# Kernel optimization log

Hardware: AMD Instinct MI355X
Metric: run time of the kernel (lower is better)

Reference implementation:

```python
import jax, jax.numpy as jnp
import numpy as np

B, H, LQ, LK, D = 2, 16, 2048, 2048, 128

def setup_inputs() -> dict:
    key = jax.random.key(0)
    k1, k2, k3 = jax.random.split(key, 3)
    q = jax.random.normal(k1, (B, H, LQ, D), dtype=jnp.float32)
    k = jax.random.normal(k2, (B, H, LK, D), dtype=jnp.float32)
    v = jax.random.normal(k3, (B, H, LK, D), dtype=jnp.float32)
    return {"q": q, "k": k, "v": v}

def reference(q, k, v):
    # scaled dot-product attention: softmax(q k^T / sqrt(D)) v
    scale = q.shape[-1] ** (-0.5)
    # scores: [B,H,Lq,Lk]
    scores = jnp.einsum('bhqd,bhkd->bhqk', q, k) * scale
    attn = jax.nn.softmax(scores, axis=-1)
    out = jnp.einsum('bhqk,bhkd->bhqd', attn, v)  # [B,H,Lq,Dv]
    return out
```

## Files before the change

kernel.cpp:

```cpp
#include <hip/hip_runtime.h>
#include <hip/hip_bf16.h>
#include <cstdint>

#define LQ_N   2048
#define LK_N   2048
#define DD     128
#define NHEADS 32
#define QBLK   128
#define KVBLK  64
#define NKV    (LK_N / KVBLK)
#define NQB    (LQ_N / QBLK)
#define SCALE  0.08838834764831845f
#define SCALE2 0.1275525003267101f

#define KTILE_BYTES (KVBLK * DD * 2)
#define WS_K_BYTES  ((size_t)NHEADS * NKV * KTILE_BYTES)
#define WS_NEED     (2 * WS_K_BYTES)

#define PSTR 72

typedef __attribute__((ext_vector_type(8)))  short bf16x8;
typedef __attribute__((ext_vector_type(4)))  float f32x4;
typedef __attribute__((ext_vector_type(16))) float f32x16;

#if __has_builtin(__builtin_amdgcn_exp2f)
#define EXP2F __builtin_amdgcn_exp2f
#else
#define EXP2F exp2f
#endif

#define MFMA32(a, b, c) __builtin_amdgcn_mfma_f32_32x32x16_bf16((a), (b), (c), 0, 0, 0)

__device__ inline unsigned short f2bf(float f) {
    union { float f; unsigned u; } x; x.f = f;
    unsigned r = (x.u + 0x7fffu + ((x.u >> 16) & 1u)) >> 16;
    return (unsigned short)r;
}

__device__ inline unsigned cvt_pk_bf16(float lo, float hi) {
    unsigned r;
    asm("v_cvt_pk_bf16_f32 %0, %1, %2" : "=v"(r) : "v"(lo), "v"(hi));
    return r;
}

__device__ inline float fmax4(float a, float b, float c, float d) {
    return fmaxf(fmaxf(a, b), fmaxf(c, d));
}

__device__ inline bf16x8 make_pfrag(float v0, float v1, float v2, float v3,
                                    float v4, float v5, float v6, float v7) {
    unsigned a0 = cvt_pk_bf16(v0, v1);
    unsigned a1 = cvt_pk_bf16(v2, v3);
    unsigned b0 = cvt_pk_bf16(v4, v5);
    unsigned b1 = cvt_pk_bf16(v6, v7);
    asm("v_permlane32_swap_b32 %0, %1" : "+v"(a0), "+v"(b0));
    asm("v_permlane32_swap_b32 %0, %1" : "+v"(a1), "+v"(b1));
    union { unsigned u[4]; bf16x8 v8; } u;
    u.u[0] = a0; u.u[1] = a1; u.u[2] = b0; u.u[3] = b1;
    return u.v8;
}

__device__ inline void gld16(const char* g, const char* l) {
    __builtin_amdgcn_global_load_lds(
        (const __attribute__((address_space(1))) unsigned int*)g,
        (__attribute__((address_space(3))) unsigned int*)l,
        16, 0, 0);
}

__global__ __launch_bounds__(256, 2)
void prep_k_kernel(const float* __restrict__ K, char* __restrict__ ws)
{
    __shared__ unsigned short kt[KVBLK * 136];
    const int tid  = threadIdx.x;
    const int kvt  = blockIdx.x;
    const int head = blockIdx.y;
    const float* Kh = K + ((size_t)head * LK_N + (size_t)kvt * KVBLK) * DD;
    #pragma unroll
    for (int i = 0; i < 4; ++i) {
        int c = tid + 256 * i;
        int r  = c >> 4;
        int c8 = c & 15;
        const float* src = Kh + (size_t)r * DD + c8 * 8;
        float4 a = *(const float4*)src;
        float4 b = *(const float4*)(src + 4);
        bf16x8 t;
        t[0] = (short)f2bf(a.x * SCALE2); t[1] = (short)f2bf(a.y * SCALE2);
        t[2] = (short)f2bf(a.z * SCALE2); t[3] = (short)f2bf(a.w * SCALE2);
        t[4] = (short)f2bf(b.x * SCALE2); t[5] = (short)f2bf(b.y * SCALE2);
        t[6] = (short)f2bf(b.z * SCALE2); t[7] = (short)f2bf(b.w * SCALE2);
        *(bf16x8*)&kt[r * 136 + c8 * 8] = t;
    }
    __syncthreads();
    char* dst = ws + ((size_t)head * NKV + kvt) * KTILE_BYTES;
    #pragma unroll
    for (int i = 0; i < 4; ++i) {
        int c = tid + 256 * i;
        int g = c >> 6;
        int r = c & 63;
        bf16x8 t = *(const bf16x8*)&kt[r * 136 + g * 8];
        *(bf16x8*)(dst + c * 16) = t;
    }
}

__global__ __launch_bounds__(256, 2)
void prep_vt_kernel(const float* __restrict__ V, char* __restrict__ ws)
{
    __shared__ unsigned short vt[DD * PSTR];
    const int tid  = threadIdx.x;
    const int kvt  = blockIdx.x;
    const int head = blockIdx.y;
    const float* Vh = V + ((size_t)head * LK_N + (size_t)kvt * KVBLK) * DD;
    #pragma unroll
    for (int i = 0; i < 8; ++i) {
        int f = tid + 256 * i;
        int r  = f >> 5;
        int c4 = f & 31;
        float4 x = *(const float4*)(Vh + (size_t)r * DD + c4 * 4);
        vt[(c4 * 4 + 0) * PSTR + r] = f2bf(x.x);
        vt[(c4 * 4 + 1) * PSTR + r] = f2bf(x.y);
        vt[(c4 * 4 + 2) * PSTR + r] = f2bf(x.z);
        vt[(c4 * 4 + 3) * PSTR + r] = f2bf(x.w);
    }
    __syncthreads();
    char* dst = ws + WS_K_BYTES + ((size_t)head * NKV + kvt) * KTILE_BYTES;
    #pragma unroll
    for (int i = 0; i < 4; ++i) {
        int c = tid + 256 * i;
        int g = c >> 7;
        int d = c & 127;
        bf16x8 t = *(const bf16x8*)&vt[d * PSTR + g * 8];
        *(bf16x8*)(dst + c * 16) = t;
    }
}

#define LOADVF(a0, a1, a2, a3, KS) { \
    a0 = *(const bf16x8*)(vtile + (((2 * (KS) + h) * 128 +  0 + l31) << 4)); \
    a1 = *(const bf16x8*)(vtile + (((2 * (KS) + h) * 128 + 32 + l31) << 4)); \
    a2 = *(const bf16x8*)(vtile + (((2 * (KS) + h) * 128 + 64 + l31) << 4)); \
    a3 = *(const bf16x8*)(vtile + (((2 * (KS) + h) * 128 + 96 + l31) << 4)); }

#define PV_ROUND(S, B, a0, a1, a2, a3) { \
    float e0 = EXP2F(S[B + 0] - m_run), e1 = EXP2F(S[B + 1] - m_run); \
    float e2 = EXP2F(S[B + 2] - m_run), e3 = EXP2F(S[B + 3] - m_run); \
    float e4 = EXP2F(S[B + 4] - m_run), e5 = EXP2F(S[B + 5] - m_run); \
    float e6 = EXP2F(S[B + 6] - m_run), e7 = EXP2F(S[B + 7] - m_run); \
    sum += ((e0 + e1) + (e2 + e3)) + ((e4 + e5) + (e6 + e7)); \
    bf16x8 pf = make_pfrag(e0, e1, e2, e3, e4, e5, e6, e7); \
    __builtin_amdgcn_s_setprio(1); \
    o_acc[0] = MFMA32(a0, pf, o_acc[0]); \
    o_acc[1] = MFMA32(a1, pf, o_acc[1]); \
    o_acc[2] = MFMA32(a2, pf, o_acc[2]); \
    o_acc[3] = MFMA32(a3, pf, o_acc[3]); \
    __builtin_amdgcn_s_setprio(0); }

__global__ __launch_bounds__(256, 2)
void attn_main_kernel(const float* __restrict__ Q, const char* __restrict__ kws,
                      const char* __restrict__ vws, float* __restrict__ O)
{
    __shared__ bf16x8 kbuf[3][KTILE_BYTES / 16];

    const int tid  = threadIdx.x;
    const int lane = tid & 63;
    const int wave = tid >> 6;
    const int l31  = lane & 31;
    const int h    = lane >> 5;

    const int bid  = blockIdx.x;
    const int sid  = (bid & 7) * (NQB * NHEADS / 8) + (bid >> 3);
    const int head = sid >> 4;
    const int qb   = sid & 15;

    const float* Qh = Q + (size_t)head * LQ_N * DD;
    float*       Oh = O + (size_t)head * LQ_N * DD;
    const char*  kt_g = kws + (size_t)head * NKV * KTILE_BYTES;
    const char*  vt_g = vws + (size_t)head * NKV * KTILE_BYTES;

    const int qrow = qb * QBLK + wave * 32 + l31;
    bf16x8 qf[8];
    {
        const float* qp = Qh + (size_t)qrow * DD + 8 * h;
        #pragma unroll
        for (int kd = 0; kd < 8; ++kd) {
            float4 a = *(const float4*)(qp + 16 * kd);
            float4 b = *(const float4*)(qp + 16 * kd + 4);
            bf16x8 t;
            t[0] = (short)f2bf(a.x); t[1] = (short)f2bf(a.y);
            t[2] = (short)f2bf(a.z); t[3] = (short)f2bf(a.w);
            t[4] = (short)f2bf(b.x); t[5] = (short)f2bf(b.y);
            t[6] = (short)f2bf(b.z); t[7] = (short)f2bf(b.w);
            qf[kd] = t;
        }
    }
    asm volatile("s_waitcnt vmcnt(0)" ::: "memory");

    f32x16 o_acc[4];
    #pragma unroll
    for (int nt = 0; nt < 4; ++nt)
        #pragma unroll
        for (int i = 0; i < 16; ++i) o_acc[nt][i] = 0.f;
    float m_run = -1e30f, l_run = 0.f;

    auto issue_k = [&](int t) {
        const char* ks = kt_g + (size_t)t * KTILE_BYTES;
        const char* kl = (const char*)&kbuf[t % 3][0];
        #pragma unroll
        for (int i = 0; i < 4; ++i) {
            int off = (tid + 256 * i) * 16;
            gld16(ks + off, kl + off);
        }
    };

    issue_k(0);
    issue_k(1);

    for (int t = 0; t < NKV; ++t) {
        const char* vtile = vt_g + (size_t)t * KTILE_BYTES;
        bf16x8 vA0, vA1, vA2, vA3, vB0, vB1, vB2, vB3;

        LOADVF(vA0, vA1, vA2, vA3, 0);

        if (t < NKV - 1) asm volatile("s_waitcnt vmcnt(8)" ::: "memory");
        else             asm volatile("s_waitcnt vmcnt(4)" ::: "memory");
        __builtin_amdgcn_s_barrier();
        __builtin_amdgcn_sched_barrier(0);

        if (t + 2 < NKV) issue_k(t + 2);

        const char* kb = (const char*)&kbuf[t % 3][0];

        f32x16 s0, s1;
        #pragma unroll
        for (int i = 0; i < 16; ++i) { s0[i] = 0.f; s1[i] = 0.f; }
        __builtin_amdgcn_s_setprio(1);
        #pragma unroll
        for (int kd = 0; kd < 8; ++kd) {
            bf16x8 kf0 = *(const bf16x8*)(kb + (((2 * kd + h) * 64 + l31) << 4));
            bf16x8 kf1 = *(const bf16x8*)(kb + (((2 * kd + h) * 64 + 32 + l31) << 4));
            s0 = MFMA32(kf0, qf[kd], s0);
            s1 = MFMA32(kf1, qf[kd], s1);
        }
        __builtin_amdgcn_s_setprio(0);

        float x0 = fmax4(s0[0],  s0[1],  s0[2],  s0[3]);
        float x1 = fmax4(s0[4],  s0[5],  s0[6],  s0[7]);
        float x2 = fmax4(s0[8],  s0[9],  s0[10], s0[11]);
        float x3 = fmax4(s0[12], s0[13], s0[14], s0[15]);
        float y0 = fmax4(s1[0],  s1[1],  s1[2],  s1[3]);
        float y1 = fmax4(s1[4],  s1[5],  s1[6],  s1[7]);
        float y2 = fmax4(s1[8],  s1[9],  s1[10], s1[11]);
        float y3 = fmax4(s1[12], s1[13], s1[14], s1[15]);
        float pm = fmaxf(fmaxf(fmaxf(x0, x1), fmaxf(x2, x3)),
                         fmaxf(fmaxf(y0, y1), fmaxf(y2, y3)));
        pm = fmaxf(pm, __shfl_xor(pm, 32));

        if (!__all(pm <= m_run + 8.0f)) {
            float mn = fmaxf(m_run, pm);
            float al = EXP2F(m_run - mn);
            m_run = mn;
            l_run *= al;
            #pragma unroll
            for (int nt = 0; nt < 4; ++nt)
                #pragma unroll
                for (int i = 0; i < 16; ++i) o_acc[nt][i] *= al;
        }

        float sum = 0.f;
        LOADVF(vB0, vB1, vB2, vB3, 1);
        PV_ROUND(s0, 0, vA0, vA1, vA2, vA3);
        LOADVF(vA0, vA1, vA2, vA3, 2);
        PV_ROUND(s0, 8, vB0, vB1, vB2, vB3);
        LOADVF(vB0, vB1, vB2, vB3, 3);
        PV_ROUND(s1, 0, vA0, vA1, vA2, vA3);
        PV_ROUND(s1, 8, vB0, vB1, vB2, vB3);

        sum += __shfl_xor(sum, 32);
        l_run += sum;
    }

    float inv = 1.0f / l_run;
    float* op = Oh + (size_t)qrow * DD;
    #pragma unroll
    for (int nt = 0; nt < 4; ++nt)
        #pragma unroll
        for (int p = 0; p < 4; ++p) {
            int dbase = 32 * nt + 8 * p + 4 * h;
            float4 w;
            w.x = o_acc[nt][4 * p + 0] * inv;
            w.y = o_acc[nt][4 * p + 1] * inv;
            w.z = o_acc[nt][4 * p + 2] * inv;
            w.w = o_acc[nt][4 * p + 3] * inv;
            *(float4*)(op + dbase) = w;
        }
}

#define KSTRIDE  136
#define VTSTRIDE 40
#define FKV 32

__global__ __launch_bounds__(256, 2)
void attn_fwd_fallback(const float* __restrict__ Q, const float* __restrict__ K,
                       const float* __restrict__ V, float* __restrict__ O)
{
    __shared__ unsigned short k_lds[FKV * KSTRIDE];
    __shared__ unsigned short vt_lds[DD * VTSTRIDE];
    __shared__ unsigned short p_lds2[4 * 16 * VTSTRIDE];

    const int tid  = threadIdx.x;
    const int lane = tid & 63;
    const int wave = tid >> 6;
    const int head = blockIdx.y;
    const int qb   = blockIdx.x;

    const float* Qh = Q + (size_t)head * LQ_N * DD;
    const float* Kh = K + (size_t)head * LK_N * DD;
    const float* Vh = V + (size_t)head * LK_N * DD;
    float*       Oh = O + (size_t)head * LQ_N * DD;

    const int r16 = lane & 15;
    const int g   = lane >> 4;

    const int qrow = qb * 64 + wave * 16 + r16;
    bf16x8 qf[4];
    {
        const float* qp = Qh + (size_t)qrow * DD + 8 * g;
        #pragma unroll
        for (int kt = 0; kt < 4; ++kt) {
            float4 a = *(const float4*)(qp + 32 * kt);
            float4 b = *(const float4*)(qp + 32 * kt + 4);
            bf16x8 t;
            t[0] = (short)f2bf(a.x * SCALE); t[1] = (short)f2bf(a.y * SCALE);
            t[2] = (short)f2bf(a.z * SCALE); t[3] = (short)f2bf(a.w * SCALE);
            t[4] = (short)f2bf(b.x * SCALE); t[5] = (short)f2bf(b.y * SCALE);
            t[6] = (short)f2bf(b.z * SCALE); t[7] = (short)f2bf(b.w * SCALE);
            qf[kt] = t;
        }
    }

    f32x4 o_acc[8];
    #pragma unroll
    for (int dt = 0; dt < 8; ++dt) o_acc[dt] = (f32x4){0.f, 0.f, 0.f, 0.f};
    float m_run[4], l_run[4];
    #pragma unroll
    for (int r = 0; r < 4; ++r) { m_run[r] = -1e30f; l_run[r] = 0.f; }

    for (int kv = 0; kv < LK_N / FKV; ++kv) {
        const float* Kt = Kh + (size_t)kv * FKV * DD;
        const float* Vt = Vh + (size_t)kv * FKV * DD;
        __syncthreads();
        #pragma unroll
        for (int i = 0; i < 4; ++i) {
            int f = tid + 256 * i;
            int row = f >> 5, colf = f & 31;
            float4 x = *(const float4*)(Kt + (size_t)row * DD + colf * 4);
            ushort4 pk;
            pk.x = f2bf(x.x); pk.y = f2bf(x.y); pk.z = f2bf(x.z); pk.w = f2bf(x.w);
            *(ushort4*)(&k_lds[row * KSTRIDE + colf * 4]) = pk;
        }
        #pragma unroll
        for (int i = 0; i < 4; ++i) {
            int f = tid + 256 * i;
            int row = f >> 5, colf = f & 31;
            float4 x = *(const float4*)(Vt + (size_t)row * DD + colf * 4);
            vt_lds[(colf * 4 + 0) * VTSTRIDE + row] = f2bf(x.x);
            vt_lds[(colf * 4 + 1) * VTSTRIDE + row] = f2bf(x.y);
            vt_lds[(colf * 4 + 2) * VTSTRIDE + row] = f2bf(x.z);
            vt_lds[(colf * 4 + 3) * VTSTRIDE + row] = f2bf(x.w);
        }
        __syncthreads();

        f32x4 s0 = (f32x4){0.f,0.f,0.f,0.f};
        f32x4 s1 = (f32x4){0.f,0.f,0.f,0.f};
        #pragma unroll
        for (int kt = 0; kt < 4; ++kt) {
            bf16x8 kf0 = *(const bf16x8*)&k_lds[(r16)      * KSTRIDE + 32 * kt + 8 * g];
            bf16x8 kf1 = *(const bf16x8*)&k_lds[(16 + r16) * KSTRIDE + 32 * kt + 8 * g];
            s0 = __builtin_amdgcn_mfma_f32_16x16x32_bf16(qf[kt], kf0, s0, 0, 0, 0);
            s1 = __builtin_amdgcn_mfma_f32_16x16x32_bf16(qf[kt], kf1, s1, 0, 0, 0);
        }

        float alpha[4];
        f32x4 p0, p1;
        #pragma unroll
        for (int r = 0; r < 4; ++r) {
            float t = fmaxf(s0[r], s1[r]);
            t = fmaxf(t, __shfl_xor(t, 1));
            t = fmaxf(t, __shfl_xor(t, 2));
            t = fmaxf(t, __shfl_xor(t, 4));
            t = fmaxf(t, __shfl_xor(t, 8));
            float mn = fmaxf(m_run[r], t);
            alpha[r] = __expf(m_run[r] - mn);
            m_run[r] = mn;
            p0[r] = __expf(s0[r] - mn);
            p1[r] = __expf(s1[r] - mn);
            float su = p0[r] + p1[r];
            su += __shfl_xor(su, 1);
            su += __shfl_xor(su, 2);
            su += __shfl_xor(su, 4);
            su += __shfl_xor(su, 8);
            l_run[r] = l_run[r] * alpha[r] + su;
        }

        unsigned short* pw = &p_lds2[wave * 16 * VTSTRIDE];
        #pragma unroll
        for (int r = 0; r < 4; ++r) {
            int row = 4 * g + r;
            pw[row * VTSTRIDE + r16]      = f2bf(p0[r]);
            pw[row * VTSTRIDE + 16 + r16] = f2bf(p1[r]);
        }
        bf16x8 pf = *(const bf16x8*)&pw[r16 * VTSTRIDE + 8 * g];

        #pragma unroll
        for (int dt = 0; dt < 8; ++dt) {
            #pragma unroll
            for (int r = 0; r < 4; ++r) o_acc[dt][r] *= alpha[r];
        }
        #pragma unroll
        for (int dt = 0; dt < 8; ++dt) {
            bf16x8 vf = *(const bf16x8*)&vt_lds[(16 * dt + r16) * VTSTRIDE + 8 * g];
            o_acc[dt] = __builtin_amdgcn_mfma_f32_16x16x32_bf16(pf, vf, o_acc[dt], 0, 0, 0);
        }
    }

    #pragma unroll
    for (int r = 0; r < 4; ++r) {
        float inv = 1.0f / l_run[r];
        int row = qb * 64 + wave * 16 + 4 * g + r;
        float* op = Oh + (size_t)row * DD + r16;
        #pragma unroll
        for (int dt = 0; dt < 8; ++dt)
            op[16 * dt] = o_acc[dt][r] * inv;
    }
}

extern "C" void kernel_launch(void* const* d_in, const int* in_sizes, int n_in,
                              void* d_out, int out_size, void* d_ws, size_t ws_size,
                              hipStream_t stream) {
    const float* q = (const float*)d_in[0];
    const float* k = (const float*)d_in[1];
    const float* v = (const float*)d_in[2];
    float* o = (float*)d_out;

    if (ws_size >= WS_NEED) {
        char* ws = (char*)d_ws;
        prep_k_kernel <<<dim3(NKV, NHEADS), 256, 0, stream>>>(k, ws);
        prep_vt_kernel<<<dim3(NKV, NHEADS), 256, 0, stream>>>(v, ws);
        attn_main_kernel<<<dim3(NQB * NHEADS), 256, 0, stream>>>(
            q, ws, ws + WS_K_BYTES, o);
    } else {
        attn_fwd_fallback<<<dim3(LQ_N / 64, NHEADS), 256, 0, stream>>>(q, k, v, o);
    }
}
```

Measured before the change: 105.0 us.

## Stage V tiles in LDS alongside K with 512-thread blocks over 256 query rows

Query block size doubles to 256 rows handled by 8 waves per 512-thread block, so each K/V tile staged in LDS is shared by twice as many waves. V tiles are now loaded asynchronously into a 4-deep LDS ring next to K instead of being read straight from global memory into registers, and the per-tile work is factored into a process lambda behind a prefetch-two-ahead loop. This cuts global/L2 traffic for V and K per query row, at the cost of 128KB of dynamic shared memory, one block per CU, and a per-launch hipFuncSetAttribute call.

Result: faster. 98.64 us (-6.1%).

```diff
diff --git a/kernel.cpp b/kernel.cpp
--- a/kernel.cpp
+++ b/kernel.cpp
@@ -6,7 +6,7 @@
 #define LK_N   2048
 #define DD     128
 #define NHEADS 32
-#define QBLK   128
+#define QBLK   256
 #define KVBLK  64
 #define NKV    (LK_N / KVBLK)
 #define NQB    (LQ_N / QBLK)
@@ -17,6 +17,9 @@
 #define WS_K_BYTES  ((size_t)NHEADS * NKV * KTILE_BYTES)
 #define WS_NEED     (2 * WS_K_BYTES)
 
+#define RING       4
+#define SMEM_MAIN  (2 * RING * KTILE_BYTES)
+
 #define PSTR 72
 
 typedef __attribute__((ext_vector_type(8)))  short bf16x8;
@@ -30,6 +33,7 @@
 #endif
 
 #define MFMA32(a, b, c) __builtin_amdgcn_mfma_f32_32x32x16_bf16((a), (b), (c), 0, 0, 0)
+#define WAITV(N) asm volatile("s_waitcnt vmcnt(" #N ")" ::: "memory")
 
 __device__ inline unsigned short f2bf(float f) {
     union { float f; unsigned u; } x; x.f = f;
@@ -133,31 +137,29 @@
     }
 }
 
-#define LOADVF(a0, a1, a2, a3, KS) { \
-    a0 = *(const bf16x8*)(vtile + (((2 * (KS) + h) * 128 +  0 + l31) << 4)); \
-    a1 = *(const bf16x8*)(vtile + (((2 * (KS) + h) * 128 + 32 + l31) << 4)); \
-    a2 = *(const bf16x8*)(vtile + (((2 * (KS) + h) * 128 + 64 + l31) << 4)); \
-    a3 = *(const bf16x8*)(vtile + (((2 * (KS) + h) * 128 + 96 + l31) << 4)); }
-
-#define PV_ROUND(S, B, a0, a1, a2, a3) { \
+#define PV_ROUND(S, B, KS) { \
     float e0 = EXP2F(S[B + 0] - m_run), e1 = EXP2F(S[B + 1] - m_run); \
     float e2 = EXP2F(S[B + 2] - m_run), e3 = EXP2F(S[B + 3] - m_run); \
     float e4 = EXP2F(S[B + 4] - m_run), e5 = EXP2F(S[B + 5] - m_run); \
     float e6 = EXP2F(S[B + 6] - m_run), e7 = EXP2F(S[B + 7] - m_run); \
     sum += ((e0 + e1) + (e2 + e3)) + ((e4 + e5) + (e6 + e7)); \
     bf16x8 pf = make_pfrag(e0, e1, e2, e3, e4, e5, e6, e7); \
+    bf16x8 vf0 = *(const bf16x8*)(vb + (((2 * (KS) + h) * 128 +  0 + l31) << 4)); \
+    bf16x8 vf1 = *(const bf16x8*)(vb + (((2 * (KS) + h) * 128 + 32 + l31) << 4)); \
+    bf16x8 vf2 = *(const bf16x8*)(vb + (((2 * (KS) + h) * 128 + 64 + l31) << 4)); \
+    bf16x8 vf3 = *(const bf16x8*)(vb + (((2 * (KS) + h) * 128 + 96 + l31) << 4)); \
     __builtin_amdgcn_s_setprio(1); \
-    o_acc[0] = MFMA32(a0, pf, o_acc[0]); \
-    o_acc[1] = MFMA32(a1, pf, o_acc[1]); \
-    o_acc[2] = MFMA32(a2, pf, o_acc[2]); \
-    o_acc[3] = MFMA32(a3, pf, o_acc[3]); \
+    o_acc[0] = MFMA32(vf0, pf, o_acc[0]); \
+    o_acc[1] = MFMA32(vf1, pf, o_acc[1]); \
+    o_acc[2] = MFMA32(vf2, pf, o_acc[2]); \
+    o_acc[3] = MFMA32(vf3, pf, o_acc[3]); \
     __builtin_amdgcn_s_setprio(0); }
 
-__global__ __launch_bounds__(256, 2)
+__global__ __launch_bounds__(512, 1)
 void attn_main_kernel(const float* __restrict__ Q, const char* __restrict__ kws,
                       const char* __restrict__ vws, float* __restrict__ O)
 {
-    __shared__ bf16x8 kbuf[3][KTILE_BYTES / 16];
+    extern __shared__ char smem[];
 
     const int tid  = threadIdx.x;
     const int lane = tid & 63;
@@ -167,8 +169,8 @@
 
     const int bid  = blockIdx.x;
     const int sid  = (bid & 7) * (NQB * NHEADS / 8) + (bid >> 3);
-    const int head = sid >> 4;
-    const int qb   = sid & 15;
+    const int head = sid >> 3;
+    const int qb   = sid & 7;
 
     const float* Qh = Q + (size_t)head * LQ_N * DD;
     float*       Oh = O + (size_t)head * LQ_N * DD;
@@ -200,33 +202,22 @@
         for (int i = 0; i < 16; ++i) o_acc[nt][i] = 0.f;
     float m_run = -1e30f, l_run = 0.f;
 
-    auto issue_k = [&](int t) {
+    auto issue_t = [&](int t) {
         const char* ks = kt_g + (size_t)t * KTILE_BYTES;
-        const char* kl = (const char*)&kbuf[t % 3][0];
-        #pragma unroll
-        for (int i = 0; i < 4; ++i) {
-            int off = (tid + 256 * i) * 16;
+        const char* vs = vt_g + (size_t)t * KTILE_BYTES;
+        const char* kl = smem + (size_t)(t & 3) * KTILE_BYTES;
+        const char* vl = smem + (size_t)(RING + (t & 3)) * KTILE_BYTES;
+        #pragma unroll
+        for (int i = 0; i < 2; ++i) {
+            int off = (tid + 512 * i) * 16;
             gld16(ks + off, kl + off);
+            gld16(vs + off, vl + off);
         }
     };
 
-    issue_k(0);
-    issue_k(1);
-
-    for (int t = 0; t < NKV; ++t) {
-        const char* vtile = vt_g + (size_t)t * KTILE_BYTES;
-        bf16x8 vA0, vA1, vA2, vA3, vB0, vB1, vB2, vB3;
-
-        LOADVF(vA0, vA1, vA2, vA3, 0);
-
-        if (t < NKV - 1) asm volatile("s_waitcnt vmcnt(8)" ::: "memory");
-        else             asm volatile("s_waitcnt vmcnt(4)" ::: "memory");
-        __builtin_amdgcn_s_barrier();
-        __builtin_amdgcn_sched_barrier(0);
-
-        if (t + 2 < NKV) issue_k(t + 2);
-
-        const char* kb = (const char*)&kbuf[t % 3][0];
+    auto process = [&](int t) {
+        const char* kb = smem + (size_t)(t & 3) * KTILE_BYTES;
+        const char* vb = smem + (size_t)(RING + (t & 3)) * KTILE_BYTES;
 
         f32x16 s0, s1;
         #pragma unroll
@@ -265,16 +256,24 @@
         }
 
         float sum = 0.f;
-        LOADVF(vB0, vB1, vB2, vB3, 1);
-        PV_ROUND(s0, 0, vA0, vA1, vA2, vA3);
-        LOADVF(vA0, vA1, vA2, vA3, 2);
-        PV_ROUND(s0, 8, vB0, vB1, vB2, vB3);
-        LOADVF(vB0, vB1, vB2, vB3, 3);
-        PV_ROUND(s1, 0, vA0, vA1, vA2, vA3);
-        PV_ROUND(s1, 8, vB0, vB1, vB2, vB3);
-
+        PV_ROUND(s0, 0, 0);
+        PV_ROUND(s0, 8, 1);
+        PV_ROUND(s1, 0, 2);
+        PV_ROUND(s1, 8, 3);
         sum += __shfl_xor(sum, 32);
         l_run += sum;
+    };
+
+    issue_t(0);
+    issue_t(1);
+
+    for (int t = 0; t < NKV; ++t) {
+        if (t < NKV - 1) WAITV(4);
+        else             WAITV(0);
+        __builtin_amdgcn_s_barrier();
+        __builtin_amdgcn_sched_barrier(0);
+        if (t + 2 < NKV) issue_t(t + 2);
+        process(t);
     }
 
     float inv = 1.0f / l_run;
@@ -440,11 +439,15 @@
     const float* v = (const float*)d_in[2];
     float* o = (float*)d_out;
 
-    if (ws_size >= WS_NEED) {
+    hipError_t attr_ok = hipFuncSetAttribute(
+        (const void*)attn_main_kernel,
+        hipFuncAttributeMaxDynamicSharedMemorySize, SMEM_MAIN);
+
+    if (ws_size >= WS_NEED && attr_ok == hipSuccess) {
         char* ws = (char*)d_ws;
         prep_k_kernel <<<dim3(NKV, NHEADS), 256, 0, stream>>>(k, ws);
         prep_vt_kernel<<<dim3(NKV, NHEADS), 256, 0, stream>>>(v, ws);
-        attn_main_kernel<<<dim3(NQB * NHEADS), 256, 0, stream>>>(
+        attn_main_kernel<<<dim3(NQB * NHEADS), 512, SMEM_MAIN, stream>>>(
             q, ws, ws + WS_K_BYTES, o);
     } else {
         attn_fwd_fallback<<<dim3(LQ_N / 64, NHEADS), 256, 0, stream>>>(q, k, v, o);
```
